# Performance work log

Measured on AMD Instinct MI355X. Metric: run time of the kernel, lower is better.

The kernel has to match this reference:

```python
import jax, jax.numpy as jnp
import numpy as np

DN = ('NCHW', 'OIHW', 'NCHW')

def conv(x, w, b, stride=1, pad=((1, 1), (1, 1))):
    y = jax.lax.conv_general_dilated(x, w, (stride, stride), pad, dimension_numbers=DN)
    return y + b[None, :, None, None]

def l2norm(x, axis):
    return x / jnp.maximum(jnp.linalg.norm(x, axis=axis, keepdims=True), 1e-12)

def groupnorm(x, g, b, groups=32, eps=1e-5):
    B, C, H, W = x.shape
    xr = x.reshape(B, groups, C // groups, H, W)
    m = xr.mean(axis=(2, 3, 4), keepdims=True)
    v = xr.var(axis=(2, 3, 4), keepdims=True)
    xr = (xr - m) / jnp.sqrt(v + eps)
    return xr.reshape(B, C, H, W) * g[None, :, None, None] + b[None, :, None, None]

def setup_inputs() -> dict:
    key = jax.random.key(0)
    ks = jax.random.split(key, 24)
    s = 0.05
    B, L, C = 8, 77, 256
    inp = {
        'images': jax.random.normal(ks[0], (B, 3, 512, 512), jnp.float32),
        'text_tokens': jax.random.randint(ks[1], (B, L), 0, 49408, jnp.int32),
        'tok512': jax.random.normal(ks[2], (B, L, 512), jnp.float32),
        # TinyImageEncoder stem (3->64->256, stride 4 total)
        'conv1_w': jax.random.normal(ks[3], (64, 3, 3, 3), jnp.float32) * s,
        'conv1_b': jnp.zeros((64,), jnp.float32),
        'conv2_w': jax.random.normal(ks[4], (C, 64, 3, 3), jnp.float32) * s,
        'conv2_b': jnp.zeros((C,), jnp.float32),
        # SpatialPosResidual2D: 1x1 convs 2->64->256 (hid = max(32, C//4) = 64)
        'sp1_w': jax.random.normal(ks[5], (64, 2, 1, 1), jnp.float32) * s,
        'sp1_b': jnp.zeros((64,), jnp.float32),
        'sp2_w': jax.random.normal(ks[6], (C, 64, 1, 1), jnp.float32) * s,
        'sp2_b': jnp.zeros((C,), jnp.float32),
        # token_proj: Linear(512, C); token_gate: Linear(C, C) + sigmoid
        'proj_w': jax.random.normal(ks[7], (512, C), jnp.float32) * s,
        'proj_b': jnp.zeros((C,), jnp.float32),
        'gate_w': jax.random.normal(ks[8], (C, C), jnp.float32) * s,
        'gate_b': jnp.zeros((C,), jnp.float32),
        # decoder: Conv(2C+1->C,3x3) + GN + ReLU + Conv(C->64,3x3) + ReLU + Conv(64->1,1x1)
        'd1_w': jax.random.normal(ks[9], (C, 2 * C + 1, 3, 3), jnp.float32) * s,
        'd1_b': jnp.zeros((C,), jnp.float32),
        'gn_g': jnp.ones((C,), jnp.float32),
        'gn_b': jnp.zeros((C,), jnp.float32),
        'd2_w': jax.random.normal(ks[10], (64, C, 3, 3), jnp.float32) * s,
        'd2_b': jnp.zeros((64,), jnp.float32),
        'd3_w': jax.random.normal(ks[11], (1, 64, 1, 1), jnp.float32) * s,
        'd3_b': jnp.zeros((1,), jnp.float32),
    }
    return inp

def reference(images, text_tokens, tok512, conv1_w, conv1_b, conv2_w, conv2_b,
              sp1_w, sp1_b, sp2_w, sp2_b, proj_w, proj_b, gate_w, gate_b,
              d1_w, d1_b, gn_g, gn_b, d2_w, d2_b, d3_w, d3_b):
    # TinyImageEncoder: two stride-2 3x3 convs -> [B, C, H/4, W/4]
    x = jax.nn.relu(conv(images, conv1_w, conv1_b, stride=2))
    x = jax.nn.relu(conv(x, conv2_w, conv2_b, stride=2))
    b, c, h, w = x.shape
    # SpatialPosResidual2D: learnable encoding of normalized x/y grid
    yy = jnp.broadcast_to(jnp.linspace(-1.0, 1.0, h, dtype=x.dtype)[None, None, :, None], (1, 1, h, w))
    xx = jnp.broadcast_to(jnp.linspace(-1.0, 1.0, w, dtype=x.dtype)[None, None, None, :], (1, 1, h, w))
    coord = jnp.concatenate([xx, yy], axis=1)  # [1, 2, h, w]
    pos = conv(jax.nn.relu(conv(coord, sp1_w, sp1_b, pad=((0, 0), (0, 0)))), sp2_w, sp2_b, pad=((0, 0), (0, 0)))
    img = x + pos
    dense = l2norm(img, axis=1)  # per-pixel L2 over channels
    # text tokens -> projected, gated, normalized
    proj = tok512 @ proj_w + proj_b                       # [B, L, C]
    tok = jax.nn.sigmoid(proj @ gate_w + gate_b) * proj
    tok = l2norm(tok, axis=-1)
    valid = (text_tokens != 0).astype(dense.dtype)        # [B, L]
    # single-head cross-modal attention: pixels attend to tokens
    v = dense.reshape(b, c, h * w).transpose(0, 2, 1)     # [B, HW, C]
    scores = jnp.einsum('bnc,blc->bnl', v, tok) * (float(c) ** -0.5)
    scores = jnp.where(valid[:, None, :] == 0, jnp.asarray(-10000.0, scores.dtype), scores)
    attn = jax.nn.softmax(scores, axis=-1)
    ctx = jnp.einsum('bnl,blc->bnc', attn, tok)           # [B, HW, C]
    ctx_map = ctx.transpose(0, 2, 1).reshape(b, c, h, w)
    # global similarity map
    wsum = jnp.maximum(valid.sum(axis=1, keepdims=True), 1.0)
    gvec = l2norm((tok * valid[:, :, None]).sum(axis=1) / wsum, axis=-1)  # [B, C]
    sim = jnp.sum(dense * gvec[:, :, None, None], axis=1, keepdims=True)  # [B, 1, h, w]
    fused = jnp.concatenate([img, ctx_map, sim], axis=1)  # [B, 2C+1, h, w]
    y = jax.nn.relu(groupnorm(conv(fused, d1_w, d1_b), gn_g, gn_b))
    y = jax.nn.relu(conv(y, d2_w, d2_b))
    y = conv(y, d3_w, d3_b, pad=((0, 0), (0, 0)))
    # bilinear upsample to input resolution (align_corners=False semantics)
    return jax.image.resize(y, (b, 1, images.shape[2], images.shape[3]), 'bilinear')
```

## Files before the change

### kernel.cpp

```cpp
#include <hip/hip_runtime.h>
#include <math.h>

typedef unsigned short u16;
typedef __attribute__((ext_vector_type(4))) unsigned short u16x4;
typedef __attribute__((ext_vector_type(8))) unsigned short u16x8;
typedef __attribute__((ext_vector_type(8))) short short8;
typedef __attribute__((ext_vector_type(4))) float f32x4;

#define BB 8
#define CC 256
#define LL 77
#define HW 16384
#define XROW 520

__device__ __forceinline__ float bf2f(u16 h) {
  return __uint_as_float(((unsigned)h) << 16);
}
__device__ __forceinline__ u16 f2bf(float f) {
  unsigned u = __float_as_uint(f);
  unsigned r = (u + 0x7fffu + ((u >> 16) & 1u)) >> 16;
  return (u16)r;
}

static const size_t OFF_XT    = 0;
static const size_t OFF_B     = 136314880;
static const size_t OFF_GVECB = 630784;
static const size_t OFF_GNSUM = 203423744;
static const size_t WS_BYTES_NEEDED = 203425792;
static const size_t OFF_Y2T = 0;
static const size_t OFF_GA  = 16777216;
static const size_t OFF_GB  = 16785408;
static const size_t OFF_Y3  = 16793600;
static const size_t WT1_BYTES = 9u * 256u * 544u * 2u;
static const size_t WT2_BYTES = 9u * 64u * 256u * 2u;

__global__ __launch_bounds__(256) void fill_kernel(float* __restrict__ out,
                                                   int n, float v) {
  int i = blockIdx.x * 256 + threadIdx.x;
  if (i < n) out[i] = v;
}

__global__ __launch_bounds__(512) void zero_gnsum(float* __restrict__ g) {
  g[threadIdx.x] = 0.f;
}

__global__ __launch_bounds__(256) void prep_wt(
    const float* __restrict__ w, u16* __restrict__ wt,
    int OC, int ICSRC, int ICPAD, int total) {
  int idx = blockIdx.x * 256 + threadIdx.x;
  if (idx >= total) return;
  int ic = idx % ICPAD;
  int oc = (idx / ICPAD) % OC;
  int kk = idx / (ICPAD * OC);
  float v = 0.f;
  if (ic < ICSRC) v = w[((size_t)oc * ICSRC + ic) * 9 + kk];
  wt[idx] = f2bf(v);
}

__global__ __launch_bounds__(256) void pos_xt(
    const float* __restrict__ sp1_w, const float* __restrict__ sp1_b,
    const float* __restrict__ sp2_w, const float* __restrict__ sp2_b,
    u16* __restrict__ xt) {
  __shared__ float hid[64 * 64];
  __shared__ u16 pv[64 * 256];
  const int tid = threadIdx.x;
  const int px0 = blockIdx.x * 64;
  #pragma unroll
  for (int i = 0; i < 16; ++i) {
    int slot = i * 256 + tid;
    int pxl = slot >> 6, h = slot & 63;
    int px = px0 + pxl;
    float xx = -1.f + (px & 127) * (2.f / 127.f);
    float yy = -1.f + (px >> 7) * (2.f / 127.f);
    hid[slot] = fmaxf(sp1_w[2 * h] * xx + sp1_w[2 * h + 1] * yy + sp1_b[h], 0.f);
  }
  float wr[64];
  #pragma unroll
  for (int q = 0; q < 16; ++q) {
    float4 v = *reinterpret_cast<const float4*>(sp2_w + tid * 64 + q * 4);
    wr[q * 4] = v.x; wr[q * 4 + 1] = v.y; wr[q * 4 + 2] = v.z; wr[q * 4 + 3] = v.w;
  }
  const float sb = sp2_b[tid];
  __syncthreads();
  for (int pxl = 0; pxl < 64; ++pxl) {
    float acc = sb;
    const float* hr = &hid[pxl * 64];
    #pragma unroll
    for (int h = 0; h < 64; ++h) acc = fmaf(wr[h], hr[h], acc);
    pv[pxl * 256 + tid] = f2bf(acc);
  }
  __syncthreads();
  for (int b = 0; b < BB; ++b) {
    u16* xb = xt + ((size_t)b * HW + px0) * XROW;
    #pragma unroll
    for (int it = 0; it < 8; ++it) {
      int slot = it * 256 + tid;
      int pxl = slot >> 5, cg = slot & 31;
      *reinterpret_cast<u16x8*>(xb + (size_t)pxl * XROW + cg * 8) =
          *reinterpret_cast<const u16x8*>(&pv[pxl * 256 + cg * 8]);
    }
  }
}

__global__ __launch_bounds__(256) void conv1_kernel(
    const float* __restrict__ in, const float* __restrict__ w,
    const float* __restrict__ bias, u16* __restrict__ x1t) {
  __shared__ float wl[27 * 64];
  __shared__ float bl[64];
  const int tid = threadIdx.x;
  const int oh = blockIdx.x;
  const int b = blockIdx.y;
  for (int i = tid; i < 27 * 64; i += 256) {
    int oc = i & 63;
    int t = i >> 6;
    wl[t * 64 + oc] = w[oc * 27 + t];
  }
  if (tid < 64) bl[tid] = bias[tid];
  __syncthreads();
  const int ow = tid;
  float acc[64];
  #pragma unroll
  for (int oc = 0; oc < 64; ++oc) acc[oc] = bl[oc];
  for (int ic = 0; ic < 3; ++ic) {
    #pragma unroll
    for (int kh = 0; kh < 3; ++kh) {
      int ih = 2 * oh + kh - 1;
      if ((unsigned)ih >= 512u) continue;
      const float* row = in + ((size_t)(b * 3 + ic) * 512 + ih) * 512;
      int iw = 2 * ow - 1;
      float v0 = (iw >= 0) ? row[iw] : 0.f;
      float v1 = row[iw + 1];
      float v2 = row[iw + 2];
      const float* wr = &wl[(ic * 3 + kh) * 192];
      #pragma unroll
      for (int oc = 0; oc < 64; ++oc)
        acc[oc] += v0 * wr[oc] + v1 * wr[64 + oc] + v2 * wr[128 + oc];
    }
  }
  u16* orow = x1t + ((size_t)b * 65536 + oh * 256 + ow) * 64;
  #pragma unroll
  for (int q = 0; q < 8; ++q) {
    u16x8 o;
    #pragma unroll
    for (int k = 0; k < 8; ++k) o[k] = f2bf(fmaxf(acc[q * 8 + k], 0.f));
    *reinterpret_cast<u16x8*>(orow + q * 8) = o;
  }
}

__global__ __launch_bounds__(256) void conv2_mfma(
    const u16* __restrict__ x1t, const u16* __restrict__ wt,
    const float* __restrict__ bias, u16* __restrict__ xt) {
  __shared__ u16 lb[15480];
  const int tid = threadIdx.x;
  const int lane = tid & 63;
  const int w = tid >> 6;
  int lin = blockIdx.x + (int)gridDim.x * blockIdx.z;
  int nwg = (int)gridDim.x * (int)gridDim.z;
  int swz = (lin & 7) * (nwg >> 3) + (lin >> 3);
  int bx = swz % (int)gridDim.x;
  int bz = swz / (int)gridDim.x;
  const int oh = bx >> 1;
  const int half = bx & 1;
  const int ow0 = half << 6;
  const int b = bz;
  const int colA = lane & 15;
  const int g = lane >> 4;
  const int oc0w = w * 64;

  f32x4 acc[4][4];
  #pragma unroll
  for (int of = 0; of < 4; ++of) {
    f32x4 bv;
    #pragma unroll
    for (int r = 0; r < 4; ++r) bv[r] = bias[oc0w + of * 16 + g * 4 + r];
    #pragma unroll
    for (int pf = 0; pf < 4; ++pf) acc[of][pf] = bv;
  }

  const u16* xb = x1t + (size_t)b * 65536 * 64;
  for (int ch = 0; ch < 2; ++ch) {
    __syncthreads();
    for (int slot = tid; slot < 1548; slot += 256) {
      int icg = slot & 3;
      int rc = slot >> 2;
      int kh, ip;
      if (rc < 192) {
        kh = rc / 64; int i = rc - kh * 64; ip = (ow0 << 1) + 2 * i;
      } else {
        int rc2 = rc - 192; kh = rc2 / 65; int j = rc2 - kh * 65;
        ip = (ow0 << 1) - 1 + 2 * j;
      }
      int ih = 2 * oh + kh - 1;
      u16x8 v = {0, 0, 0, 0, 0, 0, 0, 0};
      if ((unsigned)ih < 256u && (unsigned)ip < 256u)
        v = *reinterpret_cast<const u16x8*>(
            xb + ((size_t)(ih * 256 + ip)) * 64 + ch * 32 + icg * 8);
      *reinterpret_cast<u16x8*>(&lb[(rc * 5 + icg) << 3]) = v;
    }
    __syncthreads();
    #pragma unroll
    for (int kk = 0; kk < 9; ++kk) {
      const int kh = kk / 3, kw = kk - kh * 3;
      short8 afrag[4];
      const u16* wb = wt + ((size_t)kk * 256 + oc0w + colA) * 64 + ch * 32 + g * 8;
      #pragma unroll
      for (int of = 0; of < 4; ++of)
        afrag[of] = *reinterpret_cast<const short8*>(wb + (size_t)of * 16 * 64);
      #pragma unroll
      for (int pf = 0; pf < 4; ++pf) {
        int ow = pf * 16 + colA;
        int rc = (kw == 1) ? (kh * 64 + ow) : (192 + kh * 65 + ow + (kw >> 1));
        short8 bfrag = *reinterpret_cast<const short8*>(&lb[(rc * 5 + g) << 3]);
        #pragma unroll
        for (int of = 0; of < 4; ++of)
          acc[of][pf] = __builtin_amdgcn_mfma_f32_16x16x32_bf16(
              afrag[of], bfrag, acc[of][pf], 0, 0, 0);
      }
    }
  }
  #pragma unroll
  for (int of = 0; of < 4; ++of) {
    #pragma unroll
    for (int pf = 0; pf < 4; ++pf) {
      int px = oh * 128 + ow0 + pf * 16 + colA;
      int oc = oc0w + of * 16 + g * 4;
      u16* dst = xt + ((size_t)b * HW + px) * XROW + oc;
      u16x4 pz = *reinterpret_cast<const u16x4*>(dst);
      u16x4 o;
      #pragma unroll
      for (int r = 0; r < 4; ++r)
        o[r] = f2bf(fmaxf(acc[of][pf][r], 0.f) + bf2f(pz[r]));
      *reinterpret_cast<u16x4*>(dst) = o;
    }
  }
}

__global__ __launch_bounds__(256) void token_kernel(
    const float* __restrict__ tok512, const float* __restrict__ proj_w,
    const float* __restrict__ proj_b, const float* __restrict__ gate_w,
    const float* __restrict__ gate_b, float* __restrict__ tok_out) {
  __shared__ float t512[512];
  __shared__ float prj[256];
  __shared__ float red[4];
  int bl = blockIdx.x;
  int c = threadIdx.x;
  const float* trow = tok512 + (size_t)bl * 512;
  t512[c] = trow[c];
  t512[c + 256] = trow[c + 256];
  __syncthreads();
  float acc = proj_b[c];
  #pragma unroll 4
  for (int k = 0; k < 512; ++k) acc = fmaf(t512[k], proj_w[k * 256 + c], acc);
  prj[c] = acc;
  __syncthreads();
  float acc2 = gate_b[c];
  #pragma unroll 4
  for (int k = 0; k < 256; ++k) acc2 = fmaf(prj[k], gate_w[k * 256 + c], acc2);
  float g = 1.f / (1.f + __expf(-acc2));
  float tv = g * acc;
  float ss = tv * tv;
  #pragma unroll
  for (int off = 1; off < 64; off <<= 1) ss += __shfl_xor(ss, off);
  if ((c & 63) == 0) red[c >> 6] = ss;
  __syncthreads();
  float tot = red[0] + red[1] + red[2] + red[3];
  tok_out[(size_t)bl * 256 + c] = tv * (1.f / fmaxf(sqrtf(tot), 1e-12f));
}

__global__ __launch_bounds__(256) void gvec_kernel(
    const float* __restrict__ tok, const int* __restrict__ tokens,
    float* __restrict__ gvec) {
  __shared__ float red[4];
  int b = blockIdx.x, c = threadIdx.x;
  float s = 0.f;
  for (int l = 0; l < LL; ++l) {
    if (tokens[b * LL + l] != 0) s += tok[((size_t)b * LL + l) * 256 + c];
  }
  float ss = s * s;
  #pragma unroll
  for (int off = 1; off < 64; off <<= 1) ss += __shfl_xor(ss, off);
  if ((c & 63) == 0) red[c >> 6] = ss;
  __syncthreads();
  float tot = red[0] + red[1] + red[2] + red[3];
  gvec[b * 256 + c] = s * (1.f / fmaxf(sqrtf(tot), 1e-12f));
}

__global__ __launch_bounds__(256, 1) void attn_fused(
    u16* __restrict__ xt, const float* __restrict__ tok,
    const int* __restrict__ tokens, const float* __restrict__ gvec) {
  __shared__ u16 ltok[LL * 256];
  __shared__ u16 pl[64 * 104];
  __shared__ float lgv[256];
  __shared__ u16 lval[LL + 3];
  const int tid = threadIdx.x;
  const int b = blockIdx.y;
  const int px0 = blockIdx.x * 64;
  for (int slot = tid; slot < LL * 32; slot += 256) {
    int l = slot >> 5, cg = slot & 31;
    const float* tp = tok + ((size_t)b * LL + l) * 256 + cg * 8;
    float4 t0 = *reinterpret_cast<const float4*>(tp);
    float4 t1 = *reinterpret_cast<const float4*>(tp + 4);
    u16x8 v = {f2bf(t0.x), f2bf(t0.y), f2bf(t0.z), f2bf(t0.w),
               f2bf(t1.x), f2bf(t1.y), f2bf(t1.z), f2bf(t1.w)};
    *reinterpret_cast<u16x8*>(&ltok[l * 256 + cg * 8]) = v;
  }
  if (tid < LL) lval[tid] = (tokens[b * LL + tid] != 0) ? 1 : 0;
  lgv[tid] = gvec[b * 256 + tid];
  __syncthreads();
  const int pxl = tid >> 2;
  const int q = tid & 3;
  const int p = px0 + pxl;
  const u16* xr = xt + ((size_t)b * HW + p) * XROW;
  float s[20];
  #pragma unroll
  for (int i = 0; i < 20; ++i) s[i] = 0.f;
  float ssum = 0.f, simacc = 0.f;
  #pragma unroll 1
  for (int c0 = 0; c0 < 256; c0 += 32) {
    float x[32];
    #pragma unroll
    for (int qq = 0; qq < 4; ++qq) {
      u16x8 iv = *reinterpret_cast<const u16x8*>(xr + c0 + qq * 8);
      #pragma unroll
      for (int k = 0; k < 8; ++k) x[qq * 8 + k] = bf2f(iv[k]);
    }
    #pragma unroll
    for (int k = 0; k < 32; ++k) {
      ssum = fmaf(x[k], x[k], ssum);
      simacc = fmaf(x[k], lgv[c0 + k], simacc);
    }
    #pragma unroll
    for (int li = 0; li < 20; ++li) {
      int l = li * 4 + q;
      if (l < LL) {
        const u16* tr = &ltok[l * 256 + c0];
        float a2 = s[li];
        #pragma unroll
        for (int qq = 0; qq < 4; ++qq) {
          u16x8 tv = *reinterpret_cast<const u16x8*>(tr + qq * 8);
          #pragma unroll
          for (int k = 0; k < 8; ++k) a2 = fmaf(x[qq * 8 + k], bf2f(tv[k]), a2);
        }
        s[li] = a2;
      }
    }
  }
  const float invn = 1.f / fmaxf(sqrtf(ssum), 1e-12f);
  const float sc = invn * 0.0625f;
  float m = -1e30f;
  #pragma unroll
  for (int li = 0; li < 20; ++li) {
    int l = li * 4 + q;
    float v = (l < LL) ? (lval[l] ? s[li] * sc : -10000.f) : -1e30f;
    s[li] = v;
    m = fmaxf(m, v);
  }
  m = fmaxf(m, __shfl_xor(m, 1));
  m = fmaxf(m, __shfl_xor(m, 2));
  float sum = 0.f;
  #pragma unroll
  for (int li = 0; li < 20; ++li) {
    float e = __expf(s[li] - m);
    s[li] = e;
    sum += e;
  }
  sum += __shfl_xor(sum, 1);
  sum += __shfl_xor(sum, 2);
  const float rs = 1.f / sum;
  #pragma unroll
  for (int li = 0; li < 20; ++li) {
    int l = li * 4 + q;
    if (l < LL) pl[pxl * 104 + l] = f2bf(s[li] * rs);
  }
  if (q == 0) {
    u16x8 sv = {f2bf(simacc * invn), 0, 0, 0, 0, 0, 0, 0};
    *reinterpret_cast<u16x8*>(xt + ((size_t)b * HW + p) * XROW + 512) = sv;
  }
  __syncthreads();
  const int cbase = q * 64;
  float a[64];
  #pragma unroll
  for (int k = 0; k < 64; ++k) a[k] = 0.f;
  #pragma unroll 1
  for (int l = 0; l < LL; ++l) {
    float sl = bf2f(pl[pxl * 104 + l]);
    const u16* tr = &ltok[l * 256 + cbase];
    #pragma unroll
    for (int qq = 0; qq < 8; ++qq) {
      u16x8 tv = *reinterpret_cast<const u16x8*>(tr + qq * 8);
      #pragma unroll
      for (int k = 0; k < 8; ++k)
        a[qq * 8 + k] = fmaf(sl, bf2f(tv[k]), a[qq * 8 + k]);
    }
  }
  u16* xw = xt + ((size_t)b * HW + p) * XROW + 256 + cbase;
  #pragma unroll
  for (int qq = 0; qq < 8; ++qq) {
    u16x8 ov;
    #pragma unroll
    for (int k = 0; k < 8; ++k) ov[k] = f2bf(a[qq * 8 + k]);
    *reinterpret_cast<u16x8*>(xw + qq * 8) = ov;
  }
}

template <int CHUNKS, int XR, int OC, int OCW, bool AFFINE, bool GNST, bool RELU,
          int OROW>
__global__ __launch_bounds__(256) void convT_mfma(
    const u16* __restrict__ xt, const u16* __restrict__ wt,
    const float* __restrict__ bias, const float* __restrict__ gA,
    const float* __restrict__ gB, float* __restrict__ gnsum,
    u16* __restrict__ outT) {
  constexpr int ICPAD = CHUNKS * 32;
  constexpr int OCB = 4 * OCW;
  constexpr int NOF = OCW / 16;
  __shared__ u16 lb[7920];
  const int tid = threadIdx.x;
  const int lane = tid & 63;
  const int w = tid >> 6;
  int gx = (int)gridDim.x, gy = (int)gridDim.y;
  int lin = blockIdx.x + gx * (blockIdx.y + gy * blockIdx.z);
  int nwg = gx * gy * (int)gridDim.z;
  int swz = (lin & 7) * (nwg >> 3) + (lin >> 3);
  int bx = swz % gx;
  int rem = swz / gx;
  int by = rem % gy;
  int bz = rem / gy;
  const int oh = bx >> 1;
  const int ow0 = (bx & 1) << 6;
  const int oc0 = by * OCB + w * OCW;
  const int b = bz;
  const int colA = lane & 15;
  const int g = lane >> 4;

  f32x4 acc[NOF][4];
  #pragma unroll
  for (int of = 0; of < NOF; ++of) {
    f32x4 bv;
    #pragma unroll
    for (int r = 0; r < 4; ++r) bv[r] = bias[oc0 + of * 16 + g * 4 + r];
    #pragma unroll
    for (int pf = 0; pf < 4; ++pf) acc[of][pf] = bv;
  }

  const u16* xtb = xt + (size_t)b * HW * XR;
  for (int ch = 0; ch < CHUNKS; ++ch) {
    __syncthreads();
    #pragma unroll
    for (int it = 0; it < 4; ++it) {
      int slot = it * 256 + tid;
      if (slot < 792) {
        int icg = slot & 3;
        int rc = slot >> 2;
        int col = rc % 66;
        int row = rc / 66;
        int ih = oh + row - 1;
        int ip = ow0 - 1 + col;
        int chb = ch * 32 + icg * 8;
        u16x8 v = {0, 0, 0, 0, 0, 0, 0, 0};
        if ((unsigned)ih < 128u && (unsigned)ip < 128u && chb + 8 <= XR) {
          v = *reinterpret_cast<const u16x8*>(xtb + (size_t)(ih * 128 + ip) * XR + chb);
          if constexpr (AFFINE) {
            const float* ga = gA + b * 256 + chb;
            const float* gb2 = gB + b * 256 + chb;
            #pragma unroll
            for (int k = 0; k < 8; ++k)
              v[k] = f2bf(fmaxf(fmaf(bf2f(v[k]), ga[k], gb2[k]), 0.f));
          }
        }
        *reinterpret_cast<u16x8*>(&lb[(rc * 5 + icg) << 3]) = v;
      }
    }
    __syncthreads();
    #pragma unroll
    for (int kk = 0; kk < 9; ++kk) {
      const int kh = kk / 3, kw = kk - kh * 3;
      short8 afrag[NOF];
      const u16* wb = wt + ((size_t)kk * OC + oc0 + colA) * ICPAD + ch * 32 + g * 8;
      #pragma unroll
      for (int of = 0; of < NOF; ++of)
        afrag[of] = *reinterpret_cast<const short8*>(wb + (size_t)of * 16 * ICPAD);
      #pragma unroll
      for (int pf = 0; pf < 4; ++pf) {
        int colx = pf * 16 + colA + kw;
        short8 bfrag = *reinterpret_cast<const short8*>(
            &lb[((kh * 66 + colx) * 5 + g) << 3]);
        #pragma unroll
        for (int of = 0; of < NOF; ++of)
          acc[of][pf] = __builtin_amdgcn_mfma_f32_16x16x32_bf16(
              afrag[of], bfrag, acc[of][pf], 0, 0, 0);
      }
    }
  }
  #pragma unroll
  for (int of = 0; of < NOF; ++of) {
    float s = 0.f, ss = 0.f;
    #pragma unroll
    for (int pf = 0; pf < 4; ++pf) {
      int px = oh * 128 + ow0 + pf * 16 + colA;
      u16x4 o;
      #pragma unroll
      for (int r = 0; r < 4; ++r) {
        float v = acc[of][pf][r];
        if constexpr (RELU) v = fmaxf(v, 0.f);
        if constexpr (GNST) { s += v; ss = fmaf(v, v, ss); }
        o[r] = f2bf(v);
      }
      *reinterpret_cast<u16x4*>(
          outT + ((size_t)b * HW + px) * OROW + oc0 + of * 16 + g * 4) = o;
    }
    if constexpr (GNST) {
      #pragma unroll
      for (int off2 = 1; off2 < 16; off2 <<= 1) {
        s += __shfl_xor(s, off2);
        ss += __shfl_xor(ss, off2);
      }
      s += __shfl_xor(s, 16);
      ss += __shfl_xor(ss, 16);
      if (colA == 0 && (g & 1) == 0) {
        int grp = (oc0 + of * 16 + g * 4) >> 3;
        atomicAdd(gnsum + ((size_t)b * 32 + grp) * 2, s);
        atomicAdd(gnsum + ((size_t)b * 32 + grp) * 2 + 1, ss);
      }
    }
  }
}

__global__ __launch_bounds__(256) void gn_fin(
    const float* __restrict__ gnsum, const float* __restrict__ gg,
    const float* __restrict__ gb, float* __restrict__ gA,
    float* __restrict__ gB) {
  int b = blockIdx.x, c = threadIdx.x;
  int grp = c >> 3;
  float s = gnsum[((size_t)b * 32 + grp) * 2];
  float ss = gnsum[((size_t)b * 32 + grp) * 2 + 1];
  float m = s * (1.f / 131072.f);
  float var = ss * (1.f / 131072.f) - m * m;
  float istd = rsqrtf(var + 1e-5f);
  float a = istd * gg[c];
  gA[b * 256 + c] = a;
  gB[b * 256 + c] = gb[c] - m * a;
}

__global__ __launch_bounds__(256) void d3_kernel(
    const u16* __restrict__ y2t, const float* __restrict__ w3,
    const float* __restrict__ b3, float* __restrict__ y3) {
  int idx = blockIdx.x * 256 + threadIdx.x;
  const u16* r = y2t + (size_t)idx * 64;
  float acc = b3[0];
  #pragma unroll
  for (int cg = 0; cg < 8; ++cg) {
    u16x8 v = *reinterpret_cast<const u16x8*>(r + cg * 8);
    #pragma unroll
    for (int k = 0; k < 8; ++k) acc = fmaf(bf2f(v[k]), w3[cg * 8 + k], acc);
  }
  y3[idx] = acc;
}

__global__ __launch_bounds__(256) void upsample_kernel(
    const float* __restrict__ y3, float* __restrict__ out) {
  int idx = blockIdx.x * 256 + threadIdx.x;
  int b = idx >> 18;
  int rem = idx & 262143;
  int Y = rem >> 9, X = rem & 511;
  float sy = (Y + 0.5f) * 0.25f - 0.5f;
  float sx = (X + 0.5f) * 0.25f - 0.5f;
  float y0f = floorf(sy), x0f = floorf(sx);
  float fy = sy - y0f, fx = sx - x0f;
  int y0 = (int)y0f, x0 = (int)x0f;
  int y0c = max(y0, 0), y1c = min(y0 + 1, 127);
  int x0c = max(x0, 0), x1c = min(x0 + 1, 127);
  const float* yb = y3 + (size_t)b * HW;
  float v00 = yb[y0c * 128 + x0c], v01 = yb[y0c * 128 + x1c];
  float v10 = yb[y1c * 128 + x0c], v11 = yb[y1c * 128 + x1c];
  out[idx] = (1.f - fy) * ((1.f - fx) * v00 + fx * v01) +
             fy * ((1.f - fx) * v10 + fx * v11);
}

extern "C" void kernel_launch(void* const* d_in, const int* in_sizes, int n_in,
                              void* d_out, int out_size, void* d_ws, size_t ws_size,
                              hipStream_t stream) {
  const float* images  = (const float*)d_in[0];
  const int*   tokens  = (const int*)d_in[1];
  const float* tok512  = (const float*)d_in[2];
  const float* conv1_w = (const float*)d_in[3];
  const float* conv1_b = (const float*)d_in[4];
  const float* conv2_w = (const float*)d_in[5];
  const float* conv2_b = (const float*)d_in[6];
  const float* sp1_w   = (const float*)d_in[7];
  const float* sp1_b   = (const float*)d_in[8];
  const float* sp2_w   = (const float*)d_in[9];
  const float* sp2_b   = (const float*)d_in[10];
  const float* proj_w  = (const float*)d_in[11];
  const float* proj_b  = (const float*)d_in[12];
  const float* gate_w  = (const float*)d_in[13];
  const float* gate_b  = (const float*)d_in[14];
  const float* d1_w    = (const float*)d_in[15];
  const float* d1_b    = (const float*)d_in[16];
  const float* gn_g    = (const float*)d_in[17];
  const float* gn_b    = (const float*)d_in[18];
  const float* d2_w    = (const float*)d_in[19];
  const float* d2_b    = (const float*)d_in[20];
  const float* d3_w    = (const float*)d_in[21];
  const float* d3_b    = (const float*)d_in[22];

  float* outp = (float*)d_out;
  if (ws_size < WS_BYTES_NEEDED) {
    float v = 10000.0f + (float)(ws_size >> 20);
    fill_kernel<<<(out_size + 255) / 256, 256, 0, stream>>>(outp, out_size, v);
    return;
  }

  char* wsb = (char*)d_ws;
  u16*   xt    = (u16*)(wsb + OFF_XT);
  u16*   x1t   = (u16*)(wsb + OFF_B);
  float* tokb  = (float*)(wsb + OFF_B);
  float* gvecb = (float*)(wsb + OFF_B + OFF_GVECB);
  u16*   y1t   = (u16*)(wsb + OFF_B);
  float* gnsum = (float*)(wsb + OFF_GNSUM);
  u16*   y2t   = (u16*)(wsb + OFF_Y2T);
  float* gA    = (float*)(wsb + OFF_GA);
  float* gB    = (float*)(wsb + OFF_GB);
  float* y3    = (float*)(wsb + OFF_Y3);

  u16* wt1  = (u16*)d_out;
  u16* wt2  = (u16*)((char*)d_out + WT1_BYTES);
  u16* wtc2 = (u16*)((char*)d_out + WT1_BYTES + WT2_BYTES);

  prep_wt<<<(9 * 256 * 544 + 255) / 256, 256, 0, stream>>>(
      d1_w, wt1, 256, 513, 544, 9 * 256 * 544);
  prep_wt<<<(9 * 64 * 256 + 255) / 256, 256, 0, stream>>>(
      d2_w, wt2, 64, 256, 256, 9 * 64 * 256);
  prep_wt<<<(9 * 256 * 64 + 255) / 256, 256, 0, stream>>>(
      conv2_w, wtc2, 256, 64, 64, 9 * 256 * 64);
  zero_gnsum<<<1, 512, 0, stream>>>(gnsum);

  pos_xt<<<256, 256, 0, stream>>>(sp1_w, sp1_b, sp2_w, sp2_b, xt);
  conv1_kernel<<<dim3(256, 8), 256, 0, stream>>>(images, conv1_w, conv1_b, x1t);
  conv2_mfma<<<dim3(256, 1, 8), 256, 0, stream>>>(x1t, wtc2, conv2_b, xt);
  token_kernel<<<BB * LL, 256, 0, stream>>>(tok512, proj_w, proj_b, gate_w,
                                            gate_b, tokb);
  gvec_kernel<<<BB, 256, 0, stream>>>(tokb, tokens, gvecb);
  attn_fused<<<dim3(256, BB), 256, 0, stream>>>(xt, tokb, tokens, gvecb);
  convT_mfma<17, XROW, 256, 32, false, true, false, 256>
      <<<dim3(256, 2, 8), 256, 0, stream>>>(xt, wt1, d1_b, nullptr, nullptr,
                                            gnsum, y1t);
  gn_fin<<<8, 256, 0, stream>>>(gnsum, gn_g, gn_b, gA, gB);
  convT_mfma<8, 256, 64, 16, true, false, true, 64>
      <<<dim3(256, 1, 8), 256, 0, stream>>>(y1t, wt2, d2_b, gA, gB, nullptr, y2t);
  d3_kernel<<<512, 256, 0, stream>>>(y2t, d3_w, d3_b, y3);
  upsample_kernel<<<8192, 256, 0, stream>>>(y3, outp);
}
```

Measured before the change: 1.097 ms.

## Double-buffer LDS input tiles in conv MFMA kernel with register prefetch

The conv kernel now prefetches the next channel chunk's input tile into registers while the MFMA loop runs on the current chunk. After compute, it writes the prefetched tile (with the optional GroupNorm affine and ReLU) into a second LDS buffer, so there is one barrier per chunk instead of two. This hides global-load latency behind matrix math, but doubles LDS use and adds registers, which may lower occupancy.

Result: slower. 1.175 ms (+7.0%).

```diff
diff --git a/kernel.cpp b/kernel.cpp
--- a/kernel.cpp
+++ b/kernel.cpp
@@ -413,7 +413,7 @@
   constexpr int ICPAD = CHUNKS * 32;
   constexpr int OCB = 4 * OCW;
   constexpr int NOF = OCW / 16;
-  __shared__ u16 lb[7920];
+  __shared__ u16 lb[2][7920];
   const int tid = threadIdx.x;
   const int lane = tid & 63;
   const int w = tid >> 6;
@@ -443,11 +443,13 @@
   }
 
   const u16* xtb = xt + (size_t)b * HW * XR;
-  for (int ch = 0; ch < CHUNKS; ++ch) {
-    __syncthreads();
+  u16x8 streg[4];
+
+  auto load_regs = [&](int ch) {
     #pragma unroll
     for (int it = 0; it < 4; ++it) {
       int slot = it * 256 + tid;
+      u16x8 v = {0, 0, 0, 0, 0, 0, 0, 0};
       if (slot < 792) {
         int icg = slot & 3;
         int rc = slot >> 2;
@@ -456,10 +458,28 @@
         int ih = oh + row - 1;
         int ip = ow0 - 1 + col;
         int chb = ch * 32 + icg * 8;
-        u16x8 v = {0, 0, 0, 0, 0, 0, 0, 0};
-        if ((unsigned)ih < 128u && (unsigned)ip < 128u && chb + 8 <= XR) {
-          v = *reinterpret_cast<const u16x8*>(xtb + (size_t)(ih * 128 + ip) * XR + chb);
-          if constexpr (AFFINE) {
+        if ((unsigned)ih < 128u && (unsigned)ip < 128u && chb + 8 <= XR)
+          v = *reinterpret_cast<const u16x8*>(
+              xtb + (size_t)(ih * 128 + ip) * XR + chb);
+      }
+      streg[it] = v;
+    }
+  };
+  auto write_lds = [&](int ch, int bufi) {
+    #pragma unroll
+    for (int it = 0; it < 4; ++it) {
+      int slot = it * 256 + tid;
+      if (slot < 792) {
+        u16x8 v = streg[it];
+        if constexpr (AFFINE) {
+          int icg = slot & 3;
+          int rc = slot >> 2;
+          int col = rc % 66;
+          int row = rc / 66;
+          int ih = oh + row - 1;
+          int ip = ow0 - 1 + col;
+          int chb = ch * 32 + icg * 8;
+          if ((unsigned)ih < 128u && (unsigned)ip < 128u && chb + 8 <= XR) {
             const float* ga = gA + b * 256 + chb;
             const float* gb2 = gB + b * 256 + chb;
             #pragma unroll
@@ -467,10 +487,18 @@
               v[k] = f2bf(fmaxf(fmaf(bf2f(v[k]), ga[k], gb2[k]), 0.f));
           }
         }
-        *reinterpret_cast<u16x8*>(&lb[(rc * 5 + icg) << 3]) = v;
-      }
-    }
-    __syncthreads();
+        *reinterpret_cast<u16x8*>(&lb[bufi][((slot >> 2) * 5 + (slot & 3)) << 3]) = v;
+      }
+    }
+  };
+
+  load_regs(0);
+  write_lds(0, 0);
+  __syncthreads();
+
+  for (int ch = 0; ch < CHUNKS; ++ch) {
+    if (ch + 1 < CHUNKS) load_regs(ch + 1);
+    const u16* lbc = lb[ch & 1];
     #pragma unroll
     for (int kk = 0; kk < 9; ++kk) {
       const int kh = kk / 3, kw = kk - kh * 3;
@@ -483,14 +511,19 @@
       for (int pf = 0; pf < 4; ++pf) {
         int colx = pf * 16 + colA + kw;
         short8 bfrag = *reinterpret_cast<const short8*>(
-            &lb[((kh * 66 + colx) * 5 + g) << 3]);
+            &lbc[((kh * 66 + colx) * 5 + g) << 3]);
         #pragma unroll
         for (int of = 0; of < NOF; ++of)
           acc[of][pf] = __builtin_amdgcn_mfma_f32_16x16x32_bf16(
               afrag[of], bfrag, acc[of][pf], 0, 0, 0);
       }
     }
-  }
+    if (ch + 1 < CHUNKS) {
+      write_lds(ch + 1, (ch + 1) & 1);
+      __syncthreads();
+    }
+  }
+
   #pragma unroll
   for (int of = 0; of < NOF; ++of) {
     float s = 0.f, ss = 0.f;
```
